# Kernel optimization log

Hardware: AMD Instinct MI355X
Metric: run time of the kernel (lower is better)

The kernel has to match this reference:

```python
import jax, jax.numpy as jnp
import numpy as np

NUM_ATOMS = 100000
NUM_BONDS = 200000
MAX_NB = 6
ATOM_FDIM = 133
BOND_FDIM = 147
HIDDEN = 300
READOUT = 512
DEPTH = 6
ATOMS_PER_MOL = 25
NUM_MOLS = NUM_ATOMS // ATOMS_PER_MOL


def setup_inputs() -> dict:
    key = jax.random.key(0)
    ks = jax.random.split(key, 16)
    s = 0.02
    inp = {
        "f_atoms": jax.random.normal(ks[0], (NUM_ATOMS, ATOM_FDIM), jnp.float32),
        "f_bonds": jax.random.normal(ks[1], (NUM_BONDS, BOND_FDIM), jnp.float32),
        "a2b": jax.random.randint(ks[2], (NUM_ATOMS, MAX_NB), 0, NUM_BONDS),
        "b2a": jax.random.randint(ks[3], (NUM_BONDS,), 0, NUM_ATOMS),
        "b2revb": jax.random.randint(ks[4], (NUM_BONDS,), 0, NUM_BONDS),
        "mol_id": jnp.arange(NUM_ATOMS) // ATOMS_PER_MOL,
        # parameters (Linear: y = x @ W + b)
        "W_i": jax.random.normal(ks[5], (BOND_FDIM, HIDDEN), jnp.float32) * s,
        "b_i": jnp.zeros((HIDDEN,), jnp.float32),
        "W_h": jax.random.normal(ks[6], (HIDDEN, HIDDEN), jnp.float32) * s,
        "b_h": jnp.zeros((HIDDEN,), jnp.float32),
        "W_o": jax.random.normal(ks[7], (ATOM_FDIM + HIDDEN, HIDDEN), jnp.float32) * s,
        "b_o": jnp.zeros((HIDDEN,), jnp.float32),
        "W_fc0": jax.random.normal(ks[8], (HIDDEN, READOUT), jnp.float32) * s,
        "b_fc0": jnp.zeros((READOUT,), jnp.float32),
        "W_fc1": jax.random.normal(ks[9], (READOUT, READOUT), jnp.float32) * s,
        "b_fc1": jnp.zeros((READOUT,), jnp.float32),
        "W_last": jax.random.normal(ks[10], (READOUT, 1), jnp.float32) * s,
        "b_last": jnp.zeros((1,), jnp.float32),
    }
    return inp


def reference(f_atoms, f_bonds, W_i, b_i, W_h, b_h, W_o, b_o,
              W_fc0, b_fc0, W_fc1, b_fc1, W_last, b_last,
              a2b, b2a, b2revb, mol_id):
    relu = jax.nn.relu
    # input = W_i(f_bonds); message = relu(input)  (dropout p=0 -> identity)
    inp = f_bonds @ W_i + b_i                      # [B, H]
    message = relu(inp)
    for _ in range(DEPTH - 1):
        nei = message[a2b]                          # [A, nb, H] gather
        a_message = nei.sum(axis=1)                 # [A, H]
        rev_message = message[b2revb]               # [B, H]
        message = a_message[b2a] - rev_message      # [B, H]
        message = relu(inp + (message @ W_h + b_h))
    # final atom aggregation
    a_message = message[a2b].sum(axis=1)            # [A, H]
    a_input = jnp.concatenate([f_atoms, a_message], axis=1)
    atom_hiddens = relu(a_input @ W_o + b_o)        # [A, H]
    # molecule mean-pool (a_scope -> segment mean over mol_id)
    sums = jax.ops.segment_sum(atom_hiddens, mol_id, num_segments=NUM_MOLS)
    counts = jax.ops.segment_sum(jnp.ones((atom_hiddens.shape[0], 1), atom_hiddens.dtype),
                                 mol_id, num_segments=NUM_MOLS)
    mol_vecs = sums / jnp.maximum(counts, 1.0)      # [M, H]
    # readout MLP
    h = relu(mol_vecs @ W_fc0 + b_fc0)
    h = relu(h @ W_fc1 + b_fc1)
    out = h @ W_last + b_last                       # [M, 1]
    return out.reshape(-1)
```

## Files before the change

### kernel.cpp

```cpp
#include <hip/hip_runtime.h>

#define NATOMS 100000
#define NBONDS 200000
#define NMOLS  4000

typedef __bf16 bf16x8 __attribute__((ext_vector_type(8)));
typedef float  f32x4  __attribute__((ext_vector_type(4)));

__device__ unsigned short g_packWi [5  * 40 * 512];
__device__ unsigned short g_packWh [10 * 40 * 512];
__device__ unsigned short g_packWoT[5  * 40 * 512];
__device__ unsigned short g_packWoB[10 * 40 * 512];

__device__ __forceinline__ float bf2f(unsigned short u) {
    union { unsigned int i; float f; } c; c.i = ((unsigned int)u) << 16; return c.f;
}
__device__ __forceinline__ unsigned short f2bf(float f) {
    union { float f; unsigned int i; } c; c.f = f;
    unsigned int r = (c.i + 0x7FFFu + ((c.i >> 16) & 1u)) >> 16;
    return (unsigned short)r;
}

__global__ void pack_weights(const float* __restrict__ W_i,
                             const float* __restrict__ W_h,
                             const float* __restrict__ W_o)
{
    const int gid = blockIdx.x * blockDim.x + threadIdx.x;
    if (gid >= 1200 * 512) return;
    const int gg = gid >> 9;
    const int t  = gid & 511;
    const float* src; int K; unsigned short* dst; int lg;
    if (gg < 200)      { lg = gg;       src = W_i;             K = 147; dst = g_packWi; }
    else if (gg < 600) { lg = gg - 200; src = W_h;             K = 300; dst = g_packWh; }
    else if (gg < 800) { lg = gg - 600; src = W_o;             K = 133; dst = g_packWoT; }
    else               { lg = gg - 800; src = W_o + 133 * 300; K = 300; dst = g_packWoB; }
    const int s  = lg / 40, r = lg % 40;
    const int nh = r / 20, fr = (r % 20) >> 1, hl = r & 1;
    const int ln = t >> 3, j = t & 7;
    const int k = 32 * s + 8 * (ln >> 4) + j;
    const int n = 16 * (nh * 10 + fr) + (ln & 15);
    float val = (k < K && n < 300) ? src[k * 300 + n] : 0.f;
    unsigned short hi = f2bf(val);
    dst[(long)lg * 512 + t] = hl ? f2bf(val - bf2f(hi)) : hi;
}

__global__ __launch_bounds__(512, 4)
void gemm_mfma4(const void* __restrict__ Ap, int a16, int sel,
                const float* __restrict__ bias, const float* __restrict__ Cin,
                void* __restrict__ outR, int r16,
                unsigned short* __restrict__ outP16,
                long M, int K, int ksteps, int do_relu)
{
    __shared__ unsigned short Asm[2][128 * 32];
    __shared__ unsigned short Bsm[2][10240];

    const unsigned short* pp =
        (sel == 0) ? g_packWi : (sel == 1) ? g_packWh :
        (sel == 2) ? g_packWoT : g_packWoB;

    const int tid = threadIdx.x;
    const int wv  = tid >> 6;
    const int ln  = tid & 63;
    const int l15 = ln & 15;
    const int g   = ln >> 4;
    const int wm  = wv >> 1;
    const int wn  = wv & 1;
    const int bn  = blockIdx.x;
    const long row0 = (long)blockIdx.y * 128;

    f32x4 acc[2][5];
#pragma unroll
    for (int m = 0; m < 2; ++m)
#pragma unroll
        for (int f = 0; f < 5; ++f) acc[m][f] = (f32x4){0.f, 0.f, 0.f, 0.f};

    int aoff[2];
#pragma unroll
    for (int m = 0; m < 2; ++m) {
        const int r = wm * 32 + m * 16 + l15;
        aoff[m] = r * 32 + 8 * (g ^ ((r >> 1) & 3));
    }

    const int srow = tid >> 2, sq = tid & 3;
    const int sqs  = sq ^ ((srow >> 1) & 3);

#define STAGE_A(BUF, SS)                                                       \
    do {                                                                       \
        if (a16) {                                                             \
            const char* src = (const char*)Ap +                                \
                (row0 + srow) * (size_t)(2 * K) + (SS) * 64 + sqs * 16;        \
            char* dst = (char*)&Asm[BUF][0] + srow * 64 + sq * 16;             \
            __builtin_amdgcn_global_load_lds(                                  \
                (const __attribute__((address_space(1))) void*)src,            \
                (__attribute__((address_space(3))) void*)dst, 16, 0, 0);       \
        } else {                                                               \
            const float* A = (const float*)Ap;                                 \
            const long gr = row0 + srow;                                       \
            const int kb = (SS) * 32 + sqs * 8;                                \
            unsigned short tv[8];                                              \
            _Pragma("unroll")                                                  \
            for (int e = 0; e < 8; ++e)                                        \
                tv[e] = (gr < M && kb + e < K) ? f2bf(A[gr * (long)K + kb + e]) \
                                               : (unsigned short)0;            \
            ushort4 w0 = {tv[0], tv[1], tv[2], tv[3]};                         \
            ushort4 w1 = {tv[4], tv[5], tv[6], tv[7]};                         \
            *(ushort4*)(&Asm[BUF][0] + srow * 32 + sq * 8)     = w0;           \
            *(ushort4*)(&Asm[BUF][0] + srow * 32 + sq * 8 + 4) = w1;           \
        }                                                                      \
    } while (0)

#define STAGE_B(BUF, SS)                                                       \
    do {                                                                       \
        _Pragma("unroll")                                                      \
        for (int i = 0; i < 3; ++i) {                                          \
            const int c = i * 8 + wv;                                          \
            if (c < 20) {                                                      \
                const char* src = (const char*)pp +                            \
                    ((size_t)(SS) * 40 + bn * 20 + c) * 1024 + ln * 16;        \
                char* dst = (char*)&Bsm[BUF][0] + c * 1024 + ln * 16;          \
                __builtin_amdgcn_global_load_lds(                              \
                    (const __attribute__((address_space(1))) void*)src,        \
                    (__attribute__((address_space(3))) void*)dst, 16, 0, 0);   \
            }                                                                  \
        }                                                                      \
    } while (0)

    STAGE_A(0, 0);
    STAGE_B(0, 0);
    for (int s = 0; s < ksteps; ++s) {
        __syncthreads();
        if (s + 1 < ksteps) {
            STAGE_A((s + 1) & 1, s + 1);
            STAGE_B((s + 1) & 1, s + 1);
        }
        const unsigned short* Ab = &Asm[s & 1][0];
        const unsigned short* Bb = &Bsm[s & 1][0];
        bf16x8 av[2];
#pragma unroll
        for (int m = 0; m < 2; ++m) av[m] = *(const bf16x8*)(Ab + aoff[m]);
#pragma unroll
        for (int f = 0; f < 5; ++f) {
            const int fr = wn * 5 + f;
            bf16x8 bh = *(const bf16x8*)(Bb + (fr * 2 + 0) * 512 + ln * 8);
            bf16x8 bl = *(const bf16x8*)(Bb + (fr * 2 + 1) * 512 + ln * 8);
#pragma unroll
            for (int m = 0; m < 2; ++m) {
                acc[m][f] = __builtin_amdgcn_mfma_f32_16x16x32_bf16(av[m], bh, acc[m][f], 0, 0, 0);
                acc[m][f] = __builtin_amdgcn_mfma_f32_16x16x32_bf16(av[m], bl, acc[m][f], 0, 0, 0);
            }
        }
    }
#undef STAGE_A
#undef STAGE_B

#pragma unroll
    for (int f = 0; f < 5; ++f) {
        const int n = (bn * 10 + wn * 5 + f) * 16 + l15;
        if (n >= 300) continue;
        const float bv = bias ? bias[n] : 0.f;
#pragma unroll
        for (int m = 0; m < 2; ++m) {
#pragma unroll
            for (int rr = 0; rr < 4; ++rr) {
                const long row = row0 + wm * 32 + m * 16 + g * 4 + rr;
                if (row >= M) continue;
                float v = acc[m][f][rr] + bv;
                if (Cin) v += Cin[row * 300 + n];
                if (outP16) outP16[row * 300 + n] = f2bf(v);
                if (do_relu) v = fmaxf(v, 0.f);
                if (r16) ((unsigned short*)outR)[row * 300 + n] = f2bf(v);
                else     ((float*)outR)[row * 300 + n] = v;
            }
        }
    }
}

__global__ __launch_bounds__(256)
void gemm_flex(const float* __restrict__ A,
               const float* __restrict__ W,
               const float* __restrict__ bias,
               float* __restrict__ outR,
               int M, int K, int N, int do_relu)
{
    __shared__ float As[16][132];
    __shared__ float Bs[16][132];

    const int tid  = threadIdx.x;
    const int tx   = tid & 15;
    const int ty   = tid >> 4;
    const int row0 = blockIdx.y * 128;
    const int col0 = blockIdx.x * 128;

    float acc[8][8];
#pragma unroll
    for (int i = 0; i < 8; ++i)
#pragma unroll
        for (int j = 0; j < 8; ++j) acc[i][j] = 0.f;

    for (int k0 = 0; k0 < K; k0 += 16) {
        {
            const int c  = tid & 15;
            const int rb = tid >> 4;
#pragma unroll
            for (int i = 0; i < 8; ++i) {
                const int r  = rb + (i << 4);
                const int gr = row0 + r, gc = k0 + c;
                As[c][r] = (gr < M && gc < K) ? A[(long)gr * K + gc] : 0.f;
            }
        }
        {
            const int c  = tid & 127;
            const int rb = tid >> 7;
#pragma unroll
            for (int i = 0; i < 8; ++i) {
                const int r  = rb + (i << 1);
                const int gr = k0 + r, gc = col0 + c;
                Bs[r][c] = (gr < K && gc < N) ? W[(long)gr * N + gc] : 0.f;
            }
        }
        __syncthreads();
#pragma unroll
        for (int kk = 0; kk < 16; ++kk) {
            const float4* As4 = reinterpret_cast<const float4*>(&As[kk][0]);
            const float4* Bs4 = reinterpret_cast<const float4*>(&Bs[kk][0]);
            float4 a0 = As4[ty], a1 = As4[ty + 16];
            float4 b0 = Bs4[tx], b1 = Bs4[tx + 16];
            float av[8] = {a0.x, a0.y, a0.z, a0.w, a1.x, a1.y, a1.z, a1.w};
            float bv[8] = {b0.x, b0.y, b0.z, b0.w, b1.x, b1.y, b1.z, b1.w};
#pragma unroll
            for (int i = 0; i < 8; ++i)
#pragma unroll
                for (int j = 0; j < 8; ++j)
                    acc[i][j] = fmaf(av[i], bv[j], acc[i][j]);
        }
        __syncthreads();
    }
#pragma unroll
    for (int i = 0; i < 8; ++i) {
        const int lr = (i < 4) ? (ty * 4 + i) : (64 + ty * 4 + (i - 4));
        const int gr = row0 + lr;
        if (gr >= M) continue;
#pragma unroll
        for (int j = 0; j < 8; ++j) {
            const int lc = (j < 4) ? (tx * 4 + j) : (64 + tx * 4 + (j - 4));
            const int gc = col0 + lc;
            if (gc >= N) continue;
            float v = acc[i][j];
            if (bias) v += bias[gc];
            if (do_relu) v = fmaxf(v, 0.f);
            outR[(long)gr * N + gc] = v;
        }
    }
}

__global__ void aggregate_bf16(const unsigned short* __restrict__ src,
                               const int* __restrict__ a2b,
                               unsigned short* __restrict__ dst)
{
    const int idx = blockIdx.x * blockDim.x + threadIdx.x;
    if (idx >= NATOMS * 75) return;
    const int a = idx / 75;
    const int q = idx - a * 75;
    const int* nb = a2b + a * 6;
    float s0 = 0.f, s1 = 0.f, s2 = 0.f, s3 = 0.f;
#pragma unroll
    for (int k = 0; k < 6; ++k) {
        const ushort4 v = *reinterpret_cast<const ushort4*>(src + (long)nb[k] * 300 + (q << 2));
        s0 += bf2f(v.x); s1 += bf2f(v.y); s2 += bf2f(v.z); s3 += bf2f(v.w);
    }
    ushort4 r;
    r.x = f2bf(s0); r.y = f2bf(s1); r.z = f2bf(s2); r.w = f2bf(s3);
    *reinterpret_cast<ushort4*>(dst + ((long)idx << 2)) = r;
}

__global__ void fused_update(const unsigned short* __restrict__ t,
                             const int* __restrict__ a2b,
                             const int* __restrict__ b2a,
                             const int* __restrict__ b2revb,
                             const float* __restrict__ b_h,
                             const unsigned short* __restrict__ inp,
                             unsigned short* __restrict__ dst)
{
    const int idx = blockIdx.x * blockDim.x + threadIdx.x;
    if (idx >= NBONDS * 75) return;
    const int b = idx / 75;
    const int q = idx - b * 75;
    const long own = (long)b * 300 + (q << 2);
    const ushort4 vi = *reinterpret_cast<const ushort4*>(inp + own);
    const float4 vh = *reinterpret_cast<const float4*>(b_h + (q << 2));
    float s0 = bf2f(vi.x) + vh.x;
    float s1 = bf2f(vi.y) + vh.y;
    float s2 = bf2f(vi.z) + vh.z;
    float s3 = bf2f(vi.w) + vh.w;
    const int a = b2a[b];
    const int* nb = a2b + a * 6;
#pragma unroll
    for (int k = 0; k < 6; ++k) {
        const ushort4 v = *reinterpret_cast<const ushort4*>(t + (long)nb[k] * 300 + (q << 2));
        s0 += bf2f(v.x); s1 += bf2f(v.y); s2 += bf2f(v.z); s3 += bf2f(v.w);
    }
    {
        const ushort4 v = *reinterpret_cast<const ushort4*>(t + (long)b2revb[b] * 300 + (q << 2));
        s0 -= bf2f(v.x); s1 -= bf2f(v.y); s2 -= bf2f(v.z); s3 -= bf2f(v.w);
    }
    ushort4 o;
    o.x = f2bf(fmaxf(s0, 0.f));
    o.y = f2bf(fmaxf(s1, 0.f));
    o.z = f2bf(fmaxf(s2, 0.f));
    o.w = f2bf(fmaxf(s3, 0.f));
    *reinterpret_cast<ushort4*>(dst + own) = o;
}

__global__ void pool_kernel(const float* __restrict__ ah, float* __restrict__ mol)
{
    const int idx = blockIdx.x * blockDim.x + threadIdx.x;
    if (idx >= NMOLS * 75) return;
    const int m = idx / 75;
    const int q = idx - m * 75;
    const float* base = ah + (long)m * 25 * 300 + (q << 2);
    float s0 = 0.f, s1 = 0.f, s2 = 0.f, s3 = 0.f;
#pragma unroll
    for (int a = 0; a < 25; ++a) {
        const float4 v = *reinterpret_cast<const float4*>(base + a * 300);
        s0 += v.x; s1 += v.y; s2 += v.z; s3 += v.w;
    }
    float4 r; r.x = s0 / 25.f; r.y = s1 / 25.f; r.z = s2 / 25.f; r.w = s3 / 25.f;
    *reinterpret_cast<float4*>(mol + ((long)idx << 2)) = r;
}

__global__ void diag_kernel(float* __restrict__ out, float wsmb)
{
    const int i = blockIdx.x * blockDim.x + threadIdx.x;
    if (i < NMOLS) out[i] = (i == 0) ? wsmb : 0.f;
}

extern "C" void kernel_launch(void* const* d_in, const int* in_sizes, int n_in,
                              void* d_out, int out_size, void* d_ws, size_t ws_size,
                              hipStream_t stream)
{
    const float* f_atoms = (const float*)d_in[0];
    const float* f_bonds = (const float*)d_in[1];
    const int*   a2b     = (const int*)d_in[2];
    const int*   b2a     = (const int*)d_in[3];
    const int*   b2revb  = (const int*)d_in[4];
    const float* W_i    = (const float*)d_in[6];
    const float* b_i    = (const float*)d_in[7];
    const float* W_h    = (const float*)d_in[8];
    const float* b_h    = (const float*)d_in[9];
    const float* W_o    = (const float*)d_in[10];
    const float* b_o    = (const float*)d_in[11];
    const float* W_fc0  = (const float*)d_in[12];
    const float* b_fc0  = (const float*)d_in[13];
    const float* W_fc1  = (const float*)d_in[14];
    const float* b_fc1  = (const float*)d_in[15];
    const float* W_last = (const float*)d_in[16];
    const float* b_last = (const float*)d_in[17];
    float* out = (float*)d_out;

    if (ws_size < 240000000ull) {
        diag_kernel<<<(NMOLS + 255) / 256, 256, 0, stream>>>(out, (float)(ws_size >> 20));
        return;
    }

    const dim3 gBond(2, (NBONDS + 127) / 128);
    const dim3 gAtom(2, (NATOMS + 127) / 128);
    const int aggBlocks = (NATOMS * 75 + 255) / 256;
    const int updBlocks = (NBONDS * 75 + 255) / 256;

    pack_weights<<<(1200 * 512 + 255) / 256, 256, 0, stream>>>(W_i, W_h, W_o);

    if (ws_size >= 360000000ull) {
        unsigned short* inpB = (unsigned short*)d_ws;
        unsigned short* msgB = (unsigned short*)((char*)d_ws + 120000000);
        unsigned short* tB   = (unsigned short*)((char*)d_ws + 240000000);
        unsigned short* amB  = (unsigned short*)d_ws;
        float* tmpF = (float*)((char*)d_ws + 120000000);
        float* molF = (float*)((char*)d_ws + 240000000);
        float* h0   = molF + 2000000;
        float* h1   = molF + 5000000;

        gemm_mfma4<<<gBond, 512, 0, stream>>>(f_bonds, 0, 0, b_i, nullptr,
                                              msgB, 1, inpB, NBONDS, 147, 5, 1);
        for (int d = 0; d < 5; ++d) {
            gemm_mfma4<<<gBond, 512, 0, stream>>>(msgB, 1, 1, nullptr, nullptr,
                                                  tB, 1, nullptr, NBONDS, 300, 10, 0);
            fused_update<<<updBlocks, 256, 0, stream>>>(tB, a2b, b2a, b2revb, b_h,
                                                        inpB, msgB);
        }
        aggregate_bf16<<<aggBlocks, 256, 0, stream>>>(msgB, a2b, amB);
        gemm_mfma4<<<gAtom, 512, 0, stream>>>(f_atoms, 0, 2, nullptr, nullptr,
                                              tmpF, 0, nullptr, NATOMS, 133, 5, 0);
        gemm_mfma4<<<gAtom, 512, 0, stream>>>(amB, 1, 3, b_o, tmpF,
                                              tmpF, 0, nullptr, NATOMS, 300, 10, 1);
        pool_kernel<<<(NMOLS * 75 + 255) / 256, 256, 0, stream>>>(tmpF, molF);
        gemm_flex<<<dim3(4, 32), 256, 0, stream>>>(molF, W_fc0, b_fc0, h0, NMOLS, 300, 512, 1);
        gemm_flex<<<dim3(4, 32), 256, 0, stream>>>(h0, W_fc1, b_fc1, h1, NMOLS, 512, 512, 1);
        gemm_flex<<<dim3(1, 32), 256, 0, stream>>>(h1, W_last, b_last, out, NMOLS, 512, 1, 0);
    } else {
        unsigned short* msgB = (unsigned short*)d_ws;
        unsigned short* tB   = (unsigned short*)((char*)d_ws + 120000000);
        unsigned short* amB  = tB;
        float* tmpF = (float*)d_ws;
        float* molF = (float*)((char*)d_ws + 180000000);
        float* h0   = molF + 2000000;
        float* h1   = molF + 5000000;

        gemm_mfma4<<<gBond, 512, 0, stream>>>(f_bonds, 0, 0, b_i, nullptr,
                                              msgB, 1, nullptr, NBONDS, 147, 5, 1);
        for (int d = 0; d < 5; ++d) {
            gemm_mfma4<<<gBond, 512, 0, stream>>>(msgB, 1, 1, nullptr, nullptr,
                                                  tB, 1, nullptr, NBONDS, 300, 10, 0);
            gemm_mfma4<<<gBond, 512, 0, stream>>>(f_bonds, 0, 0, b_i, nullptr,
                                                  msgB, 1, nullptr, NBONDS, 147, 5, 0);
            fused_update<<<updBlocks, 256, 0, stream>>>(tB, a2b, b2a, b2revb, b_h,
                                                        msgB, msgB);
        }
        aggregate_bf16<<<aggBlocks, 256, 0, stream>>>(msgB, a2b, amB);
        gemm_mfma4<<<gAtom, 512, 0, stream>>>(f_atoms, 0, 2, nullptr, nullptr,
                                              tmpF, 0, nullptr, NATOMS, 133, 5, 0);
        gemm_mfma4<<<gAtom, 512, 0, stream>>>(amB, 1, 3, b_o, tmpF,
                                              tmpF, 0, nullptr, NATOMS, 300, 10, 1);
        pool_kernel<<<(NMOLS * 75 + 255) / 256, 256, 0, stream>>>(tmpF, molF);
        gemm_flex<<<dim3(4, 32), 256, 0, stream>>>(molF, W_fc0, b_fc0, h0, NMOLS, 300, 512, 1);
        gemm_flex<<<dim3(4, 32), 256, 0, stream>>>(h0, W_fc1, b_fc1, h1, NMOLS, 512, 512, 1);
        gemm_flex<<<dim3(1, 32), 256, 0, stream>>>(h1, W_last, b_last, out, NMOLS, 512, 1, 0);
    }
}
```

Baseline: 2.778 ms.

## Compute full 320-wide N per block and stage bf16 epilogue through LDS

The GEMM now covers all 300 output columns in one block (10 fragments per wave), so each A row tile is loaded once instead of by two column blocks. B is single-buffered and loaded per k-step with an extra barrier. The bf16 output path writes results into LDS and then stores coalesced 8-byte chunks, applying ReLU on the packed bf16 values. This raises register and LDS use (about 56KB), which may lower occupancy, and removes the double buffering of B.

```diff
diff --git a/kernel.cpp b/kernel.cpp
--- a/kernel.cpp
+++ b/kernel.cpp
@@ -19,6 +19,11 @@
     union { float f; unsigned int i; } c; c.f = f;
     unsigned int r = (c.i + 0x7FFFu + ((c.i >> 16) & 1u)) >> 16;
     return (unsigned short)r;
+}
+__device__ __forceinline__ unsigned int relu2(unsigned int u) {
+    if (u & 0x00008000u) u &= 0xFFFF0000u;
+    if (u & 0x80000000u) u &= 0x0000FFFFu;
+    return u;
 }
 
 __global__ void pack_weights(const float* __restrict__ W_i,
@@ -45,14 +50,16 @@
 }
 
 __global__ __launch_bounds__(512, 4)
-void gemm_mfma4(const void* __restrict__ Ap, int a16, int sel,
+void gemm_mfma5(const void* __restrict__ Ap, int a16, int sel,
                 const float* __restrict__ bias, const float* __restrict__ Cin,
                 void* __restrict__ outR, int r16,
                 unsigned short* __restrict__ outP16,
                 long M, int K, int ksteps, int do_relu)
 {
-    __shared__ unsigned short Asm[2][128 * 32];
-    __shared__ unsigned short Bsm[2][10240];
+    __shared__ unsigned long long lds8[57344 / 8];
+    unsigned short* Asm0 = (unsigned short*)lds8;
+    unsigned short* Bsm  = (unsigned short*)lds8 + 8192;
+    unsigned short* ep   = (unsigned short*)lds8;
 
     const unsigned short* pp =
         (sel == 0) ? g_packWi : (sel == 1) ? g_packWh :
@@ -65,14 +72,13 @@
     const int g   = ln >> 4;
     const int wm  = wv >> 1;
     const int wn  = wv & 1;
-    const int bn  = blockIdx.x;
-    const long row0 = (long)blockIdx.y * 128;
-
-    f32x4 acc[2][5];
+    const long row0 = (long)blockIdx.x * 128;
+
+    f32x4 acc[2][10];
 #pragma unroll
     for (int m = 0; m < 2; ++m)
 #pragma unroll
-        for (int f = 0; f < 5; ++f) acc[m][f] = (f32x4){0.f, 0.f, 0.f, 0.f};
+        for (int f = 0; f < 10; ++f) acc[m][f] = (f32x4){0.f, 0.f, 0.f, 0.f};
 
     int aoff[2];
 #pragma unroll
@@ -88,8 +94,8 @@
     do {                                                                       \
         if (a16) {                                                             \
             const char* src = (const char*)Ap +                                \
-                (row0 + srow) * (size_t)(2 * K) + (SS) * 64 + sqs * 16;        \
-            char* dst = (char*)&Asm[BUF][0] + srow * 64 + sq * 16;             \
+                (row0 + srow) * (size_t)600 + (SS) * 64 + sqs * 16;            \
+            char* dst = (char*)Asm0 + (BUF) * 8192 + srow * 64 + sq * 16;      \
             __builtin_amdgcn_global_load_lds(                                  \
                 (const __attribute__((address_space(1))) void*)src,            \
                 (__attribute__((address_space(3))) void*)dst, 16, 0, 0);       \
@@ -104,72 +110,97 @@
                                                : (unsigned short)0;            \
             ushort4 w0 = {tv[0], tv[1], tv[2], tv[3]};                         \
             ushort4 w1 = {tv[4], tv[5], tv[6], tv[7]};                         \
-            *(ushort4*)(&Asm[BUF][0] + srow * 32 + sq * 8)     = w0;           \
-            *(ushort4*)(&Asm[BUF][0] + srow * 32 + sq * 8 + 4) = w1;           \
+            *(ushort4*)(Asm0 + (BUF) * 4096 + srow * 32 + sq * 8)     = w0;    \
+            *(ushort4*)(Asm0 + (BUF) * 4096 + srow * 32 + sq * 8 + 4) = w1;    \
         }                                                                      \
     } while (0)
 
-#define STAGE_B(BUF, SS)                                                       \
+#define STAGE_B(SS)                                                            \
     do {                                                                       \
         _Pragma("unroll")                                                      \
-        for (int i = 0; i < 3; ++i) {                                          \
-            const int c = i * 8 + wv;                                          \
-            if (c < 20) {                                                      \
-                const char* src = (const char*)pp +                            \
-                    ((size_t)(SS) * 40 + bn * 20 + c) * 1024 + ln * 16;        \
-                char* dst = (char*)&Bsm[BUF][0] + c * 1024 + ln * 16;          \
-                __builtin_amdgcn_global_load_lds(                              \
-                    (const __attribute__((address_space(1))) void*)src,        \
-                    (__attribute__((address_space(3))) void*)dst, 16, 0, 0);   \
-            }                                                                  \
+        for (int i = 0; i < 5; ++i) {                                          \
+            const char* src = (const char*)pp + (size_t)(SS) * 40960           \
+                              + i * 8192 + tid * 16;                           \
+            char* dst = (char*)Bsm + i * 8192 + tid * 16;                      \
+            __builtin_amdgcn_global_load_lds(                                  \
+                (const __attribute__((address_space(1))) void*)src,            \
+                (__attribute__((address_space(3))) void*)dst, 16, 0, 0);       \
         }                                                                      \
     } while (0)
 
     STAGE_A(0, 0);
-    STAGE_B(0, 0);
     for (int s = 0; s < ksteps; ++s) {
+        STAGE_B(s);
+        if (s + 1 < ksteps) STAGE_A((s + 1) & 1, s + 1);
         __syncthreads();
-        if (s + 1 < ksteps) {
-            STAGE_A((s + 1) & 1, s + 1);
-            STAGE_B((s + 1) & 1, s + 1);
-        }
-        const unsigned short* Ab = &Asm[s & 1][0];
-        const unsigned short* Bb = &Bsm[s & 1][0];
+        const unsigned short* Ab = Asm0 + (s & 1) * 4096;
         bf16x8 av[2];
 #pragma unroll
         for (int m = 0; m < 2; ++m) av[m] = *(const bf16x8*)(Ab + aoff[m]);
 #pragma unroll
-        for (int f = 0; f < 5; ++f) {
-            const int fr = wn * 5 + f;
-            bf16x8 bh = *(const bf16x8*)(Bb + (fr * 2 + 0) * 512 + ln * 8);
-            bf16x8 bl = *(const bf16x8*)(Bb + (fr * 2 + 1) * 512 + ln * 8);
+        for (int f = 0; f < 10; ++f) {
+            const int ch = wn * 20 + f * 2;
+            bf16x8 bh = *(const bf16x8*)(Bsm + (ch + 0) * 512 + ln * 8);
+            bf16x8 bl = *(const bf16x8*)(Bsm + (ch + 1) * 512 + ln * 8);
 #pragma unroll
             for (int m = 0; m < 2; ++m) {
                 acc[m][f] = __builtin_amdgcn_mfma_f32_16x16x32_bf16(av[m], bh, acc[m][f], 0, 0, 0);
                 acc[m][f] = __builtin_amdgcn_mfma_f32_16x16x32_bf16(av[m], bl, acc[m][f], 0, 0, 0);
             }
         }
+        __syncthreads();
     }
 #undef STAGE_A
 #undef STAGE_B
 
-#pragma unroll
-    for (int f = 0; f < 5; ++f) {
-        const int n = (bn * 10 + wn * 5 + f) * 16 + l15;
-        if (n >= 300) continue;
-        const float bv = bias ? bias[n] : 0.f;
-#pragma unroll
-        for (int m = 0; m < 2; ++m) {
-#pragma unroll
-            for (int rr = 0; rr < 4; ++rr) {
-                const long row = row0 + wm * 32 + m * 16 + g * 4 + rr;
-                if (row >= M) continue;
-                float v = acc[m][f][rr] + bv;
-                if (Cin) v += Cin[row * 300 + n];
-                if (outP16) outP16[row * 300 + n] = f2bf(v);
-                if (do_relu) v = fmaxf(v, 0.f);
-                if (r16) ((unsigned short*)outR)[row * 300 + n] = f2bf(v);
-                else     ((float*)outR)[row * 300 + n] = v;
+    if (r16) {
+        for (int p = 0; p < 2; ++p) {
+            if (p) __syncthreads();
+            if ((wm >> 1) == p) {
+                const int rbase = (wm & 1) * 32;
+#pragma unroll
+                for (int f = 0; f < 10; ++f) {
+                    const int n = (wn * 10 + f) * 16 + l15;
+                    if (n >= 300) continue;
+                    const float bv = bias ? bias[n] : 0.f;
+#pragma unroll
+                    for (int m = 0; m < 2; ++m)
+#pragma unroll
+                        for (int rr = 0; rr < 4; ++rr) {
+                            const int rl = rbase + m * 16 + g * 4 + rr;
+                            ep[rl * 304 + n] = f2bf(acc[m][f][rr] + bv);
+                        }
+                }
+            }
+            __syncthreads();
+            for (int c = tid; c < 4800; c += 512) {
+                const int row = c / 75, off = c - row * 75;
+                const long grow = row0 + p * 64 + row;
+                if (grow >= M) continue;
+                uint2 v = *(const uint2*)(ep + row * 304 + off * 4);
+                if (outP16)
+                    *(uint2*)(outP16 + grow * 300 + off * 4) = v;
+                if (do_relu) { v.x = relu2(v.x); v.y = relu2(v.y); }
+                *(uint2*)((unsigned short*)outR + grow * 300 + off * 4) = v;
+            }
+        }
+    } else {
+#pragma unroll
+        for (int f = 0; f < 10; ++f) {
+            const int n = (wn * 10 + f) * 16 + l15;
+            if (n >= 300) continue;
+            const float bv = bias ? bias[n] : 0.f;
+#pragma unroll
+            for (int m = 0; m < 2; ++m) {
+#pragma unroll
+                for (int rr = 0; rr < 4; ++rr) {
+                    const long row = row0 + wm * 32 + m * 16 + g * 4 + rr;
+                    if (row >= M) continue;
+                    float v = acc[m][f][rr] + bv;
+                    if (Cin) v += Cin[row * 300 + n];
+                    if (do_relu) v = fmaxf(v, 0.f);
+                    ((float*)outR)[row * 300 + n] = v;
+                }
             }
         }
     }
@@ -362,8 +393,8 @@
         return;
     }
 
-    const dim3 gBond(2, (NBONDS + 127) / 128);
-    const dim3 gAtom(2, (NATOMS + 127) / 128);
+    const int gBond = (NBONDS + 127) / 128;
+    const int gAtom = (NATOMS + 127) / 128;
     const int aggBlocks = (NATOMS * 75 + 255) / 256;
     const int updBlocks = (NBONDS * 75 + 255) / 256;
 
@@ -379,18 +410,18 @@
         float* h0   = molF + 2000000;
         float* h1   = molF + 5000000;
 
-        gemm_mfma4<<<gBond, 512, 0, stream>>>(f_bonds, 0, 0, b_i, nullptr,
+        gemm_mfma5<<<gBond, 512, 0, stream>>>(f_bonds, 0, 0, b_i, nullptr,
                                               msgB, 1, inpB, NBONDS, 147, 5, 1);
         for (int d = 0; d < 5; ++d) {
-            gemm_mfma4<<<gBond, 512, 0, stream>>>(msgB, 1, 1, nullptr, nullptr,
+            gemm_mfma5<<<gBond, 512, 0, stream>>>(msgB, 1, 1, nullptr, nullptr,
                                                   tB, 1, nullptr, NBONDS, 300, 10, 0);
             fused_update<<<updBlocks, 256, 0, stream>>>(tB, a2b, b2a, b2revb, b_h,
                                                         inpB, msgB);
         }
         aggregate_bf16<<<aggBlocks, 256, 0, stream>>>(msgB, a2b, amB);
-        gemm_mfma4<<<gAtom, 512, 0, stream>>>(f_atoms, 0, 2, nullptr, nullptr,
+        gemm_mfma5<<<gAtom, 512, 0, stream>>>(f_atoms, 0, 2, nullptr, nullptr,
                                               tmpF, 0, nullptr, NATOMS, 133, 5, 0);
-        gemm_mfma4<<<gAtom, 512, 0, stream>>>(amB, 1, 3, b_o, tmpF,
+        gemm_mfma5<<<gAtom, 512, 0, stream>>>(amB, 1, 3, b_o, tmpF,
                                               tmpF, 0, nullptr, NATOMS, 300, 10, 1);
         pool_kernel<<<(NMOLS * 75 + 255) / 256, 256, 0, stream>>>(tmpF, molF);
         gemm_flex<<<dim3(4, 32), 256, 0, stream>>>(molF, W_fc0, b_fc0, h0, NMOLS, 300, 512, 1);
@@ -405,20 +436,20 @@
         float* h0   = molF + 2000000;
         float* h1   = molF + 5000000;
 
-        gemm_mfma4<<<gBond, 512, 0, stream>>>(f_bonds, 0, 0, b_i, nullptr,
+        gemm_mfma5<<<gBond, 512, 0, stream>>>(f_bonds, 0, 0, b_i, nullptr,
                                               msgB, 1, nullptr, NBONDS, 147, 5, 1);
         for (int d = 0; d < 5; ++d) {
-            gemm_mfma4<<<gBond, 512, 0, stream>>>(msgB, 1, 1, nullptr, nullptr,
+            gemm_mfma5<<<gBond, 512, 0, stream>>>(msgB, 1, 1, nullptr, nullptr,
                                                   tB, 1, nullptr, NBONDS, 300, 10, 0);
-            gemm_mfma4<<<gBond, 512, 0, stream>>>(f_bonds, 0, 0, b_i, nullptr,
+            gemm_mfma5<<<gBond, 512, 0, stream>>>(f_bonds, 0, 0, b_i, nullptr,
                                                   msgB, 1, nullptr, NBONDS, 147, 5, 0);
             fused_update<<<updBlocks, 256, 0, stream>>>(tB, a2b, b2a, b2revb, b_h,
                                                         msgB, msgB);
         }
         aggregate_bf16<<<aggBlocks, 256, 0, stream>>>(msgB, a2b, amB);
-        gemm_mfma4<<<gAtom, 512, 0, stream>>>(f_atoms, 0, 2, nullptr, nullptr,
+        gemm_mfma5<<<gAtom, 512, 0, stream>>>(f_atoms, 0, 2, nullptr, nullptr,
                                               tmpF, 0, nullptr, NATOMS, 133, 5, 0);
-        gemm_mfma4<<<gAtom, 512, 0, stream>>>(amB, 1, 3, b_o, tmpF,
+        gemm_mfma5<<<gAtom, 512, 0, stream>>>(amB, 1, 3, b_o, tmpF,
                                               tmpF, 0, nullptr, NATOMS, 300, 10, 1);
         pool_kernel<<<(NMOLS * 75 + 255) / 256, 256, 0, stream>>>(tmpF, molF);
         gemm_flex<<<dim3(4, 32), 256, 0, stream>>>(molF, W_fc0, b_fc0, h0, NMOLS, 300, 512, 1);
```

Measured after the change: 2.317 ms, median of 3. -16.6%, faster.
